# Performance work log

Measured on AMD Instinct MI355X. Metric: run time of the kernel, lower is better.

The kernel has to match this reference:

```python
import jax, jax.numpy as jnp
import numpy as np
import math

NUM_CLASSES = 80
IOU_LOSS_THRESH = 0.5
ANCHORS = [
    np.array([[12, 16], [19, 36], [40, 28]], dtype=np.float32),
    np.array([[36, 75], [76, 55], [72, 146]], dtype=np.float32),
    np.array([[142, 110], [192, 243], [459, 401]], dtype=np.float32),
]


def decode(conv, anchors, stride, num_class):
    B, S = conv.shape[0], conv.shape[1]
    A = anchors.shape[0]
    conv = conv.reshape(B, S, S, A, 5 + num_class)
    dxdy = conv[..., 0:2]
    dwdh = conv[..., 2:4]
    dconf = conv[..., 4:5]
    dprob = conv[..., 5:]
    r = jnp.arange(S, dtype=conv.dtype)
    # matches torch: offset[..., 0] varies along dim2, offset[..., 1] along dim1
    offset = jnp.stack([jnp.broadcast_to(r[None, :], (S, S)),
                        jnp.broadcast_to(r[:, None], (S, S))], axis=-1)
    offset = offset[None, :, :, None, :]  # (1,S,S,1,2)
    pred_xy = (jax.nn.sigmoid(dxdy) + offset) * stride
    pred_wh = jnp.exp(dwdh) * jnp.asarray(anchors)  # (A,2) broadcast
    return jnp.concatenate([pred_xy, pred_wh,
                            jax.nn.sigmoid(dconf), jax.nn.sigmoid(dprob)], axis=-1)


def _to_corners(b):
    return jnp.concatenate([b[..., :2] - b[..., 2:] * 0.5,
                            b[..., :2] + b[..., 2:] * 0.5], axis=-1)


def bbox_ciou(boxes1, boxes2):
    b1 = _to_corners(boxes1)
    b2 = _to_corners(boxes2)
    b1 = jnp.concatenate([jnp.minimum(b1[..., :2], b1[..., 2:]),
                          jnp.maximum(b1[..., :2], b1[..., 2:])], axis=-1)
    b2 = jnp.concatenate([jnp.minimum(b2[..., :2], b2[..., 2:]),
                          jnp.maximum(b2[..., :2], b2[..., 2:])], axis=-1)
    area1 = (b1[..., 2] - b1[..., 0]) * (b1[..., 3] - b1[..., 1])
    area2 = (b2[..., 2] - b2[..., 0]) * (b2[..., 3] - b2[..., 1])
    lu = jnp.maximum(b1[..., :2], b2[..., :2])
    rd = jnp.minimum(b1[..., 2:], b2[..., 2:])
    inter = jnp.maximum(rd - lu, 0.0)
    inter_area = inter[..., 0] * inter[..., 1]
    union = area1 + area2 - inter_area
    iou = inter_area / (union + 1e-9)
    enc_lu = jnp.minimum(b1[..., :2], b2[..., :2])
    enc_rd = jnp.maximum(b1[..., 2:], b2[..., 2:])
    enc_wh = enc_rd - enc_lu
    c2 = enc_wh[..., 0] ** 2 + enc_wh[..., 1] ** 2
    p2 = (boxes1[..., 0] - boxes2[..., 0]) ** 2 + (boxes1[..., 1] - boxes2[..., 1]) ** 2
    atan1 = jnp.arctan(boxes1[..., 2] / (boxes1[..., 3] + 1e-9))
    atan2 = jnp.arctan(boxes2[..., 2] / (boxes2[..., 3] + 1e-9))
    v = 4.0 * (atan1 - atan2) ** 2 / (math.pi ** 2)
    a = v / (1.0 - iou + v)
    return iou - p2 / c2 - a * v


def bbox_iou(boxes1, boxes2):
    area1 = boxes1[..., 2] * boxes1[..., 3]
    area2 = boxes2[..., 2] * boxes2[..., 3]
    b1 = _to_corners(boxes1)
    b2 = _to_corners(boxes2)
    lu = jnp.maximum(b1[..., :2], b2[..., :2])
    rd = jnp.minimum(b1[..., 2:], b2[..., 2:])
    inter = jnp.maximum(rd - lu, 0.0)
    inter_area = inter[..., 0] * inter[..., 1]
    union = area1 + area2 - inter_area
    return inter_area / union


def loss_layer(conv, pred, label, bboxes, stride, num_class, iou_loss_thresh):
    B, S = conv.shape[0], conv.shape[1]
    input_size = float(stride * S)
    pred_xywh = pred[..., 0:4]
    pred_conf = pred[..., 4:5]
    pred_prob = pred[..., 5:]
    label_xywh = label[..., 0:4]
    respond_bbox = label[..., 4:5]
    label_prob = label[..., 5:]

    ciou = bbox_ciou(pred_xywh, label_xywh)[..., None]  # (B,S,S,3,1)
    bbox_loss_scale = 2.0 - label_xywh[..., 2:3] * label_xywh[..., 3:4] / input_size ** 2
    ciou_loss = respond_bbox * bbox_loss_scale * (1.0 - ciou)

    prob_pos = label_prob * (-jnp.log(pred_prob + 1e-9))
    prob_neg = (1.0 - label_prob) * (-jnp.log(1.0 - pred_prob + 1e-9))
    prob_loss = respond_bbox * (prob_pos + prob_neg)

    iou = bbox_iou(pred_xywh[:, :, :, :, None, :],
                   bboxes[:, None, None, None, :, :])  # (B,S,S,3,70)
    max_iou = jnp.max(iou, axis=-1, keepdims=True)
    respond_bgd = (1.0 - respond_bbox) * (max_iou < iou_loss_thresh).astype(pred.dtype)
    pos_loss = respond_bbox * (-jnp.log(pred_conf + 1e-9))
    neg_loss = respond_bgd * (-jnp.log(1.0 - pred_conf + 1e-9))
    conf_loss = pos_loss + neg_loss

    ciou_loss = ciou_loss.sum(axis=(1, 2, 3, 4)).mean()
    conf_loss = conf_loss.sum(axis=(1, 2, 3, 4)).mean()
    prob_loss = prob_loss.sum(axis=(1, 2, 3, 4)).mean()
    return ciou_loss, conf_loss, prob_loss


def setup_inputs() -> dict:
    key = jax.random.key(0)
    ks = jax.random.split(key, 7)
    B, NC = 16, NUM_CLASSES
    C = 3 * (5 + NC)
    inp = {
        'conv_lbbox': jax.random.normal(ks[0], (B, 19, 19, C), jnp.float32),
        'conv_mbbox': jax.random.normal(ks[1], (B, 38, 38, C), jnp.float32),
        'conv_sbbox': jax.random.normal(ks[2], (B, 76, 76, C), jnp.float32),
        'label_sbbox': jax.random.uniform(ks[3], (B, 76, 76, 3, 5 + NC), jnp.float32),
        'label_mbbox': jax.random.uniform(ks[4], (B, 38, 38, 3, 5 + NC), jnp.float32),
        'label_lbbox': jax.random.uniform(ks[5], (B, 19, 19, 3, 5 + NC), jnp.float32),
        'true_bboxes': jax.random.uniform(ks[6], (B, 70, 4), jnp.float32, 1.0, 600.0),
    }
    return inp


def reference(conv_lbbox, conv_mbbox, conv_sbbox, label_sbbox, label_mbbox,
              label_lbbox, true_bboxes):
    nc, thr = NUM_CLASSES, IOU_LOSS_THRESH
    pred_s = decode(conv_sbbox, ANCHORS[0], 8, nc)
    pred_m = decode(conv_mbbox, ANCHORS[1], 16, nc)
    pred_l = decode(conv_lbbox, ANCHORS[2], 32, nc)
    s_ciou, s_conf, s_prob = loss_layer(conv_sbbox, pred_s, label_sbbox, true_bboxes, 8, nc, thr)
    m_ciou, m_conf, m_prob = loss_layer(conv_mbbox, pred_m, label_mbbox, true_bboxes, 16, nc, thr)
    l_ciou, l_conf, l_prob = loss_layer(conv_lbbox, pred_l, label_lbbox, true_bboxes, 32, nc, thr)
    ciou_loss = s_ciou + m_ciou + l_ciou
    conf_loss = s_conf + m_conf + l_conf
    prob_loss = s_prob + m_prob + l_prob
    all_loss = ciou_loss + conf_loss + prob_loss
    return (all_loss, ciou_loss, conf_loss, prob_loss)
```

## Files before the change

kernel.cpp:

```cpp
#include <hip/hip_runtime.h>
#include <math.h>

#define CH 85

static constexpr int RS = 16 * 76 * 76 * 3;
static constexpr int RM = 16 * 38 * 38 * 3;
static constexpr int RL = 16 * 19 * 19 * 3;

static constexpr int ES = RS * CH, EM = RM * CH, EL = RL * CH;
static constexpr int FS = ES / 4, FM = EM / 4, FL = EL / 4;

static constexpr int CHUNK = 4096;
static constexpr int NBS = (FS + CHUNK - 1) / CHUNK;
static constexpr int NBM = (FM + CHUNK - 1) / CHUNK;
static constexpr int NBL = (FL + CHUNK - 1) / CHUNK;
static constexpr int NBCE = NBS + NBM + NBL;

static constexpr int QS = RS / 256;
static constexpr int QM = (RM + 255) / 256;
static constexpr int QL = (RL + 255) / 256;
static constexpr int NQ = QS + QM + QL;

static constexpr int NBLK = NBCE + NQ;

__constant__ float c_anchors[18] = {
    12.f, 16.f, 19.f, 36.f, 40.f, 28.f,
    36.f, 75.f, 76.f, 55.f, 72.f, 146.f,
    142.f, 110.f, 192.f, 243.f, 459.f, 401.f
};

__device__ __forceinline__ float fast_rcp(float x) { return __builtin_amdgcn_rcpf(x); }
__device__ __forceinline__ float sigm(float x)     { return fast_rcp(1.f + __expf(-x)); }
__device__ __forceinline__ float softplusf(float x) {
    return fmaxf(x, 0.f) + __logf(1.f + __expf(-fabsf(x)));
}

__global__ __launch_bounds__(256) void yolo_main(
    const float* __restrict__ conv_l, const float* __restrict__ conv_m,
    const float* __restrict__ conv_s, const float* __restrict__ lab_s,
    const float* __restrict__ lab_m, const float* __restrict__ lab_l,
    const float* __restrict__ tb, float* __restrict__ pb)
{
    int blk = blockIdx.x;

    if (blk < NBCE) {
        const float* cbase; const float* lbase; int E; int q;
        if (blk < NBS)            { q = blk;              cbase = conv_s; lbase = lab_s; E = ES; }
        else if (blk < NBS + NBM) { q = blk - NBS;        cbase = conv_m; lbase = lab_m; E = EM; }
        else                      { q = blk - NBS - NBM;  cbase = conv_l; lbase = lab_l; E = EL; }

        int e = (q * CHUNK + (int)threadIdx.x) * 4;
        unsigned r = (unsigned)e / 85u;
        unsigned c = (unsigned)e - r * 85u;

        float acc = 0.f;

        #pragma unroll
        for (int g = 0; g < 4; ++g) {
            float4 cv[4], lv[4];
            float  rsp[4];
            unsigned cc[4];
            int eloc = e; unsigned rr = r, ch = c;
            #pragma unroll
            for (int it = 0; it < 4; ++it) {
                cc[it] = ch;
                if (eloc < E) {
                    cv[it]  = *reinterpret_cast<const float4*>(cbase + eloc);
                    lv[it]  = *reinterpret_cast<const float4*>(lbase + eloc);
                    rsp[it] = lbase[rr * 85u + 4u];
                } else {
                    cv[it] = make_float4(0.f, 0.f, 0.f, 0.f);
                    lv[it] = make_float4(0.f, 0.f, 0.f, 0.f);
                    rsp[it] = 0.f;
                }
                eloc += 1024; rr += 12u; ch += 4u;
                if (ch >= 85u) { ch -= 85u; ++rr; }
            }
            e = eloc; r = rr; c = ch;

            #pragma unroll
            for (int it = 0; it < 4; ++it) {
                float xs[4] = {cv[it].x, cv[it].y, cv[it].z, cv[it].w};
                float ls[4] = {lv[it].x, lv[it].y, lv[it].z, lv[it].w};
                #pragma unroll
                for (int d = 0; d < 4; ++d) {
                    unsigned cd = cc[it] + (unsigned)d;
                    float w = (cd - 5u < 80u) ? rsp[it] : 0.f;
                    float x = xs[d], l = ls[d];
                    acc = fmaf(w, softplusf(x) - l * x, acc);
                }
            }
        }

        for (int off = 32; off > 0; off >>= 1) acc += __shfl_down(acc, off);
        __shared__ float red[4];
        int lane = threadIdx.x & 63, wv = threadIdx.x >> 6;
        if (lane == 0) red[wv] = acc;
        __syncthreads();
        if (threadIdx.x == 0)
            pb[2 * NQ + blk] = red[0] + red[1] + red[2] + red[3];

    } else {
        int qb = blk - NBCE;
        const float* conv; const float* lab;
        int S; float stride; int ao; int r0; int nrec_scale;
        if (qb < QS)           { conv = conv_s; lab = lab_s; S = 76; stride = 8.f;  ao = 0;  r0 = qb * 256;              nrec_scale = RS; }
        else if (qb < QS + QM) { conv = conv_m; lab = lab_m; S = 38; stride = 16.f; ao = 6;  r0 = (qb - QS) * 256;       nrec_scale = RM; }
        else                   { conv = conv_l; lab = lab_l; S = 19; stride = 32.f; ao = 12; r0 = (qb - QS - QM) * 256;  nrec_scale = RL; }

        float ciou_acc = 0.f, conf_acc = 0.f;
        int t = threadIdx.x;
        int rec = r0 + t;
        if (rec < nrec_scale) {
            unsigned rl = (unsigned)rec;
            unsigned a = rl % 3u; unsigned qq = rl / 3u;
            unsigned j = qq % (unsigned)S; qq /= (unsigned)S;
            unsigned i = qq % (unsigned)S; unsigned b = qq / (unsigned)S;

            const float* cp = conv + (size_t)rec * CH;
            const float* lp = lab  + (size_t)rec * CH;
            float c0 = cp[0], c1 = cp[1], c2v = cp[2], c3 = cp[3], c4 = cp[4];
            float lx = lp[0], ly = lp[1], lw = lp[2], lh = lp[3], resp = lp[4];

            float px = (sigm(c0) + (float)j) * stride;
            float py = (sigm(c1) + (float)i) * stride;
            float pw = __expf(c2v) * c_anchors[ao + 2 * a];
            float ph = __expf(c3)  * c_anchors[ao + 2 * a + 1];

            float hx = 0.5f * pw, hy = 0.5f * ph;
            float b1x1 = px - hx, b1y1 = py - hy, b1x2 = px + hx, b1y2 = py + hy;
            float hlx = 0.5f * lw, hly = 0.5f * lh;
            float b2x1 = lx - hlx, b2y1 = ly - hly, b2x2 = lx + hlx, b2y2 = ly + hly;

            float area1 = (b1x2 - b1x1) * (b1y2 - b1y1);
            float area2 = (b2x2 - b2x1) * (b2y2 - b2y1);
            float lux = fmaxf(b1x1, b2x1), luy = fmaxf(b1y1, b2y1);
            float rdx = fminf(b1x2, b2x2), rdy = fminf(b1y2, b2y2);
            float iw = fmaxf(rdx - lux, 0.f), ih = fmaxf(rdy - luy, 0.f);
            float inter = iw * ih;
            float uni = area1 + area2 - inter;
            float iou = inter / (uni + 1e-9f);

            float encw = fmaxf(b1x2, b2x2) - fminf(b1x1, b2x1);
            float ench = fmaxf(b1y2, b2y2) - fminf(b1y1, b2y1);
            float cc2 = encw * encw + ench * ench;
            float dx = px - lx, dy = py - ly;
            float p2 = dx * dx + dy * dy;
            float at1 = atanf(pw / (ph + 1e-9f));
            float at2 = atanf(lw / (lh + 1e-9f));
            float dat = at1 - at2;
            const float FOUR_OVER_PI2 = 0.40528473456935109f;
            float v = FOUR_OVER_PI2 * dat * dat;
            float al = v / (1.f - iou + v);
            float ciou = iou - p2 / cc2 - al * v;
            float bscale = 2.f - lw * lh * (1.f / (608.f * 608.f));
            ciou_acc = resp * bscale * (1.f - ciou);

            const float* tbp = tb + (size_t)b * 70 * 4;
            float parea = pw * ph;
            float maxiou = 0.f;
            for (int n = 0; n < 70; n++) {
                float tx = tbp[4 * n], ty = tbp[4 * n + 1];
                float tw = tbp[4 * n + 2], th = tbp[4 * n + 3];
                float tx1 = tx - 0.5f * tw, ty1 = ty - 0.5f * th;
                float tx2 = tx + 0.5f * tw, ty2 = ty + 0.5f * th;
                float ix1 = fmaxf(b1x1, tx1), iy1 = fmaxf(b1y1, ty1);
                float ix2 = fminf(b1x2, tx2), iy2 = fminf(b1y2, ty2);
                float iiw = fmaxf(ix2 - ix1, 0.f), iih = fmaxf(iy2 - iy1, 0.f);
                float ia = iiw * iih;
                float u = parea + tw * th - ia;
                maxiou = fmaxf(maxiou, ia * fast_rcp(u));
            }
            float rbgd = (1.f - resp) * (maxiou < 0.5f ? 1.f : 0.f);
            float spc = softplusf(c4);
            conf_acc = resp * (spc - c4) + rbgd * spc;
        }

        for (int off = 32; off > 0; off >>= 1) {
            ciou_acc += __shfl_down(ciou_acc, off);
            conf_acc += __shfl_down(conf_acc, off);
        }
        __shared__ float red2[4][2];
        int lane = threadIdx.x & 63, wv = threadIdx.x >> 6;
        if (lane == 0) { red2[wv][0] = ciou_acc; red2[wv][1] = conf_acc; }
        __syncthreads();
        if (threadIdx.x == 0) {
            pb[qb]      = red2[0][0] + red2[1][0] + red2[2][0] + red2[3][0];
            pb[NQ + qb] = red2[0][1] + red2[1][1] + red2[2][1] + red2[3][1];
        }
    }
}

__global__ __launch_bounds__(256) void finalize_k(const float* __restrict__ pb,
                                                  float* __restrict__ out)
{
    double s0 = 0.0, s1 = 0.0, s2 = 0.0;
    for (int i = threadIdx.x; i < NQ; i += 256) {
        s0 += (double)pb[i];
        s1 += (double)pb[NQ + i];
    }
    for (int i = threadIdx.x; i < NBCE; i += 256) {
        s2 += (double)pb[2 * NQ + i];
    }
    for (int off = 32; off > 0; off >>= 1) {
        s0 += __shfl_down(s0, off);
        s1 += __shfl_down(s1, off);
        s2 += __shfl_down(s2, off);
    }
    __shared__ double rd[4][3];
    int lane = threadIdx.x & 63, wv = threadIdx.x >> 6;
    if (lane == 0) { rd[wv][0] = s0; rd[wv][1] = s1; rd[wv][2] = s2; }
    __syncthreads();
    if (threadIdx.x == 0) {
        float ci = (float)((rd[0][0] + rd[1][0] + rd[2][0] + rd[3][0]) / 16.0);
        float co = (float)((rd[0][1] + rd[1][1] + rd[2][1] + rd[3][1]) / 16.0);
        float pr = (float)((rd[0][2] + rd[1][2] + rd[2][2] + rd[3][2]) / 16.0);
        out[0] = ci + co + pr;
        out[1] = ci;
        out[2] = co;
        out[3] = pr;
    }
}

extern "C" void kernel_launch(void* const* d_in, const int* in_sizes, int n_in,
                              void* d_out, int out_size, void* d_ws, size_t ws_size,
                              hipStream_t stream) {
    const float* conv_l = (const float*)d_in[0];
    const float* conv_m = (const float*)d_in[1];
    const float* conv_s = (const float*)d_in[2];
    const float* lab_s  = (const float*)d_in[3];
    const float* lab_m  = (const float*)d_in[4];
    const float* lab_l  = (const float*)d_in[5];
    const float* tb     = (const float*)d_in[6];
    float* pb  = (float*)d_ws;
    float* out = (float*)d_out;

    yolo_main<<<NBLK, 256, 0, stream>>>(conv_l, conv_m, conv_s,
                                        lab_s, lab_m, lab_l, tb, pb);
    finalize_k<<<1, 256, 0, stream>>>(pb, out);
}
```

Baseline: 283.8 us.

## Stage per-record responsibility in LDS and double per-block chunk size

Each cross-entropy block now loads the responsibility value of every record it covers once into shared memory, instead of each thread doing a scattered global load per float4. The chunk per block is doubled, which halves the block count and doubles the unrolled loop. Out-of-range loads are clamped to the last valid float4 and masked, so the loads no longer sit behind a branch. This adds a __syncthreads, more registers per thread and fewer blocks, which can lower occupancy.

```diff
diff --git a/kernel.cpp b/kernel.cpp
--- a/kernel.cpp
+++ b/kernel.cpp
@@ -10,7 +10,7 @@
 static constexpr int ES = RS * CH, EM = RM * CH, EL = RL * CH;
 static constexpr int FS = ES / 4, FM = EM / 4, FL = EL / 4;
 
-static constexpr int CHUNK = 4096;
+static constexpr int CHUNK = 8192;
 static constexpr int NBS = (FS + CHUNK - 1) / CHUNK;
 static constexpr int NBM = (FM + CHUNK - 1) / CHUNK;
 static constexpr int NBL = (FL + CHUNK - 1) / CHUNK;
@@ -49,45 +49,44 @@
         else if (blk < NBS + NBM) { q = blk - NBS;        cbase = conv_m; lbase = lab_m; E = EM; }
         else                      { q = blk - NBS - NBM;  cbase = conv_l; lbase = lab_l; E = EL; }
 
-        int e = (q * CHUNK + (int)threadIdx.x) * 4;
-        unsigned r = (unsigned)e / 85u;
-        unsigned c = (unsigned)e - r * 85u;
-
+        int e_first = q * (CHUNK * 4);
+        int e_lastp = min(E, e_first + CHUNK * 4);
+        unsigned rf = (unsigned)e_first / 85u;
+        unsigned rl = (unsigned)(e_lastp - 1) / 85u;
+        int nrec_blk = (int)(rl - rf) + 1;
+
+        __shared__ float s_resp[388];
+        for (int t = threadIdx.x; t < nrec_blk; t += 256)
+            s_resp[t] = lbase[(size_t)(rf + (unsigned)t) * 85u + 4u];
+        __syncthreads();
+
+        int f40 = q * CHUNK + (int)threadIdx.x;
         float acc = 0.f;
 
         #pragma unroll
-        for (int g = 0; g < 4; ++g) {
+        for (int g = 0; g < 8; ++g) {
             float4 cv[4], lv[4];
-            float  rsp[4];
-            unsigned cc[4];
-            int eloc = e; unsigned rr = r, ch = c;
+            unsigned rr[4], cc[4], vld[4];
             #pragma unroll
-            for (int it = 0; it < 4; ++it) {
-                cc[it] = ch;
-                if (eloc < E) {
-                    cv[it]  = *reinterpret_cast<const float4*>(cbase + eloc);
-                    lv[it]  = *reinterpret_cast<const float4*>(lbase + eloc);
-                    rsp[it] = lbase[rr * 85u + 4u];
-                } else {
-                    cv[it] = make_float4(0.f, 0.f, 0.f, 0.f);
-                    lv[it] = make_float4(0.f, 0.f, 0.f, 0.f);
-                    rsp[it] = 0.f;
-                }
-                eloc += 1024; rr += 12u; ch += 4u;
-                if (ch >= 85u) { ch -= 85u; ++rr; }
+            for (int u = 0; u < 4; ++u) {
+                int e = (f40 + (g * 4 + u) * 256) << 2;
+                vld[u] = (e < E) ? 1u : 0u;
+                int es = min(e, E - 4);
+                cv[u] = *reinterpret_cast<const float4*>(cbase + es);
+                lv[u] = *reinterpret_cast<const float4*>(lbase + es);
+                unsigned r = (unsigned)es / 85u;
+                rr[u] = r; cc[u] = (unsigned)es - r * 85u;
             }
-            e = eloc; r = rr; c = ch;
-
             #pragma unroll
-            for (int it = 0; it < 4; ++it) {
-                float xs[4] = {cv[it].x, cv[it].y, cv[it].z, cv[it].w};
-                float ls[4] = {lv[it].x, lv[it].y, lv[it].z, lv[it].w};
+            for (int u = 0; u < 4; ++u) {
+                float resp = s_resp[rr[u] - rf];
+                resp = vld[u] ? resp : 0.f;
+                float xs[4] = {cv[u].x, cv[u].y, cv[u].z, cv[u].w};
+                float ls[4] = {lv[u].x, lv[u].y, lv[u].z, lv[u].w};
                 #pragma unroll
                 for (int d = 0; d < 4; ++d) {
-                    unsigned cd = cc[it] + (unsigned)d;
-                    float w = (cd - 5u < 80u) ? rsp[it] : 0.f;
-                    float x = xs[d], l = ls[d];
-                    acc = fmaf(w, softplusf(x) - l * x, acc);
+                    float w = (cc[u] + (unsigned)d - 5u < 80u) ? resp : 0.f;
+                    acc = fmaf(w, softplusf(xs[d]) - ls[d] * xs[d], acc);
                 }
             }
         }
@@ -109,11 +108,10 @@
         else                   { conv = conv_l; lab = lab_l; S = 19; stride = 32.f; ao = 12; r0 = (qb - QS - QM) * 256;  nrec_scale = RL; }
 
         float ciou_acc = 0.f, conf_acc = 0.f;
-        int t = threadIdx.x;
-        int rec = r0 + t;
+        int rec = r0 + (int)threadIdx.x;
         if (rec < nrec_scale) {
-            unsigned rl = (unsigned)rec;
-            unsigned a = rl % 3u; unsigned qq = rl / 3u;
+            unsigned rl2 = (unsigned)rec;
+            unsigned a = rl2 % 3u; unsigned qq = rl2 / 3u;
             unsigned j = qq % (unsigned)S; qq /= (unsigned)S;
             unsigned i = qq % (unsigned)S; unsigned b = qq / (unsigned)S;
 
```

After: 279.0 us. No clear change (-1.7%).
